# Kernel tuning notes

Measured on AMD Instinct MI355X. Metric: run time of the kernel, lower is better.

## Reference

```python
import jax, jax.numpy as jnp
import numpy as np

B, T, E, H = 2, 2048, 1024, 16
D = E // H  # head_dim = 64


def setup_inputs() -> dict:
    key = jax.random.key(0)
    ks = jax.random.split(key, 9)
    s = 0.02
    x = jax.random.normal(ks[0], (B, T, E), dtype=jnp.float32)
    # additive causal mask, broadcastable to (B, H, T, T)
    causal = jnp.tril(jnp.ones((T, T), dtype=bool))
    uni_causal_mask = jnp.where(causal, 0.0, -1e9).astype(jnp.float32)[None, None]
    # torch Linear weights are (out_features, in_features); out = H*D, in = D
    Wq = jax.random.normal(ks[1], (H * D, D), dtype=jnp.float32) * s
    bq = jax.random.normal(ks[2], (H * D,), dtype=jnp.float32) * s
    Wk = jax.random.normal(ks[3], (H * D, D), dtype=jnp.float32) * s
    bk = jax.random.normal(ks[4], (H * D,), dtype=jnp.float32) * s
    Wv = jax.random.normal(ks[5], (H * D, D), dtype=jnp.float32) * s
    bv = jax.random.normal(ks[6], (H * D,), dtype=jnp.float32) * s
    Wp = jax.random.normal(ks[7], (E, E), dtype=jnp.float32) * s
    bp = jax.random.normal(ks[8], (E,), dtype=jnp.float32) * s
    return {"x": x, "uni_causal_mask": uni_causal_mask,
            "Wq": Wq, "bq": bq, "Wk": Wk, "bk": bk,
            "Wv": Wv, "bv": bv, "Wp": Wp, "bp": bp}


def _per_head_proj(xh, W, b):
    # xh: (B, T, H, D). Original code projects each head's D-dim slice with
    # Linear(D, H*D) and get_head_dim keeps only the diagonal block i for
    # head i, i.e. each head uses W[i*D:(i+1)*D, :] and b[i*D:(i+1)*D].
    W3 = W.reshape(H, D, D)  # (H, out D, in D)
    b2 = b.reshape(H, D)
    y = jnp.einsum('bthi,hoi->bhto', xh, W3) + b2[None, :, None, :]
    return y  # (B, H, T, D)


def reference(x, uni_causal_mask, Wq, bq, Wk, bk, Wv, bv, Wp, bp):
    b, t, e = x.shape
    xh = x.reshape(b, t, H, D)
    q = _per_head_proj(xh, Wq, bq)  # (B,H,T,D)
    k = _per_head_proj(xh, Wk, bk)
    v = _per_head_proj(xh, Wv, bv)
    scale = D ** (-0.5)
    attn = jnp.einsum('bhtd,bhsd->bhts', (q * scale).astype(jnp.float32),
                      k.astype(jnp.float32))
    attn = attn + uni_causal_mask
    attn = jax.nn.softmax(attn, axis=-1).astype(x.dtype)
    out = jnp.einsum('bhts,bhsd->bhtd', attn, v)
    out = out.transpose(0, 2, 1, 3).reshape(b, t, e)
    return out @ Wp.T + bp
```

## Files before the change

### kernel.cpp

```cpp
#include <hip/hip_runtime.h>

typedef __attribute__((ext_vector_type(4))) float f32x4;
typedef __attribute__((ext_vector_type(8))) __bf16 bf16x8;
typedef __attribute__((ext_vector_type(4))) unsigned short us4;
typedef __attribute__((ext_vector_type(8))) unsigned short us8;

#define DEVI static __device__ __forceinline__

constexpr int T_ = 2048, E_ = 1024, H_ = 16, D_ = 64;
#define QSCALE (0.125f * 1.44269504088896f)

DEVI unsigned short f2b(float f) {
  union { __bf16 b; unsigned short u; } c; c.b = (__bf16)f; return c.u;
}

DEVI unsigned pkw(float a, float b) {
  union { __bf16 h[2]; unsigned u; } c;
  c.h[0] = (__bf16)a; c.h[1] = (__bf16)b; return c.u;
}

#if __has_builtin(__builtin_amdgcn_exp2f)
DEVI float fexp2(float x) { return __builtin_amdgcn_exp2f(x); }
#else
DEVI float fexp2(float x) { return __expf(x * 0.69314718056f); }
#endif

DEVI f32x4 mfma16(bf16x8 a, bf16x8 b, f32x4 c) {
  return __builtin_amdgcn_mfma_f32_16x16x32_bf16(a, b, c, 0, 0, 0);
}

__launch_bounds__(256)
__global__ void cvt_kernel(const float* __restrict__ Wq,
                           const float* __restrict__ Wk,
                           const float* __restrict__ Wv,
                           const float* __restrict__ Wp,
                           unsigned short* __restrict__ wqb,
                           unsigned short* __restrict__ wkb,
                           unsigned short* __restrict__ wvb,
                           unsigned short* __restrict__ wpb)
{
  int blk = blockIdx.x;
  const float* src; unsigned short* dst; float s = 1.0f;
  if (blk < 64)       { src = Wq; dst = wqb; s = QSCALE; }
  else if (blk < 128) { src = Wk; dst = wkb; blk -= 64; }
  else if (blk < 192) { src = Wv; dst = wvb; blk -= 128; }
  else                { src = Wp; dst = wpb; blk -= 192; }
  int i = blk * 256 + threadIdx.x;
  float4 v = *(const float4*)(src + (size_t)i * 4);
  us4 o; o[0] = f2b(v.x * s); o[1] = f2b(v.y * s); o[2] = f2b(v.z * s); o[3] = f2b(v.w * s);
  *(us4*)(dst + (size_t)i * 4) = o;
}

__launch_bounds__(256)
__global__ void qkv_kernel(const float* __restrict__ x,
                           const unsigned short* __restrict__ wqb,
                           const float* __restrict__ bq,
                           const unsigned short* __restrict__ wkb,
                           const float* __restrict__ bk,
                           const unsigned short* __restrict__ wvb,
                           const float* __restrict__ bv,
                           unsigned short* __restrict__ qo,
                           unsigned short* __restrict__ ko,
                           unsigned short* __restrict__ vto)
{
  const int bh = blockIdx.x;
  const int b  = bh >> 4;
  const int h  = bh & (H_ - 1);
  const int t0 = blockIdx.y * 128;
  __shared__ unsigned short Xl[128][72];
  const int tid = threadIdx.x;

  #pragma unroll
  for (int p = 0; p < 8; ++p) {
    int idx = p * 256 + tid;
    int row = idx >> 4, c4 = idx & 15;
    float4 v = *(const float4*)(x + ((size_t)(b * T_ + t0 + row)) * E_ + h * 64 + c4 * 4);
    us4 o; o[0] = f2b(v.x); o[1] = f2b(v.y); o[2] = f2b(v.z); o[3] = f2b(v.w);
    *(us4*)&Xl[row][c4 * 4] = o;
  }
  __syncthreads();

  const int w = tid >> 6, lane = tid & 63, lo = lane & 15, g = lane >> 4;
  const int tl0 = w * 32;

  bf16x8 xb[2][2];
  #pragma unroll
  for (int tt = 0; tt < 2; ++tt)
    #pragma unroll
    for (int kd = 0; kd < 2; ++kd)
      xb[tt][kd] = *(const bf16x8*)&Xl[tl0 + tt * 16 + lo][kd * 32 + g * 8];

  #pragma unroll
  for (int tsel = 0; tsel < 2; ++tsel) {
    const float* bias = tsel ? bk : bq;
    unsigned short* outp = tsel ? ko : qo;
    const unsigned short* wsrc = (tsel ? wkb : wqb) + (size_t)h * 4096;
    const float bs = tsel ? 1.0f : QSCALE;
    #pragma unroll
    for (int ot = 0; ot < 4; ++ot) {
      bf16x8 a0 = *(const bf16x8*)(wsrc + (ot * 16 + lo) * 64 + g * 8);
      bf16x8 a1 = *(const bf16x8*)(wsrc + (ot * 16 + lo) * 64 + 32 + g * 8);
      float4 bv4 = *(const float4*)(bias + h * 64 + ot * 16 + g * 4);
      float bb[4] = {bv4.x * bs, bv4.y * bs, bv4.z * bs, bv4.w * bs};
      #pragma unroll
      for (int tt = 0; tt < 2; ++tt) {
        f32x4 acc = {0.f, 0.f, 0.f, 0.f};
        acc = mfma16(a0, xb[tt][0], acc);
        acc = mfma16(a1, xb[tt][1], acc);
        int tg = t0 + tl0 + tt * 16 + lo;
        us4 pk;
        #pragma unroll
        for (int r = 0; r < 4; ++r) pk[r] = f2b(acc[r] + bb[r]);
        *(us4*)(outp + ((size_t)(bh * T_ + tg)) * 64 + ot * 16 + g * 4) = pk;
      }
    }
  }

  {
    const unsigned short* wsrc2 = wvb + (size_t)h * 4096;
    #pragma unroll
    for (int rt = 0; rt < 2; ++rt) {
      bf16x8 a0 = *(const bf16x8*)&Xl[tl0 + rt * 16 + lo][g * 8];
      bf16x8 a1 = *(const bf16x8*)&Xl[tl0 + rt * 16 + lo][32 + g * 8];
      #pragma unroll
      for (int ct = 0; ct < 4; ++ct) {
        bf16x8 b0 = *(const bf16x8*)(wsrc2 + (ct * 16 + lo) * 64 + g * 8);
        bf16x8 b1 = *(const bf16x8*)(wsrc2 + (ct * 16 + lo) * 64 + 32 + g * 8);
        f32x4 acc = {0.f, 0.f, 0.f, 0.f};
        acc = mfma16(a0, b0, acc);
        acc = mfma16(a1, b1, acc);
        int d = ct * 16 + lo;
        float bvs = bv[h * 64 + d];
        int tg = t0 + tl0 + rt * 16 + g * 4;
        us4 pk;
        #pragma unroll
        for (int r = 0; r < 4; ++r) pk[r] = f2b(acc[r] + bvs);
        *(us4*)(vto + ((size_t)(bh * 64 + d)) * T_ + tg) = pk;
      }
    }
  }
}

__launch_bounds__(256)
__global__ void flash_kernel(const unsigned short* __restrict__ q,
                             const unsigned short* __restrict__ kk_,
                             const unsigned short* __restrict__ vt,
                             unsigned short* __restrict__ ao)
{
  const int bh = blockIdx.x;
  const int b = bh >> 4, h = bh & 15;
  const int qt = 31 - blockIdx.y;
  const int t0 = qt * 64;
  __shared__ unsigned short Kl[2][64][64];
  __shared__ unsigned short Vl[3][64][64];
  const int tid = threadIdx.x, w = tid >> 6, lane = tid & 63, lo = lane & 15, g = lane >> 4;
  const int rs = lo & 7;

  const int srow = tid >> 3, sgi = tid & 7;
  const int khalf = (srow >> 2) & 1;
  const int gsrc = (srow >> 3) ^ (khalf << 1);
  const int prow = khalf * 16 + gsrc * 4 + (srow & 3);
  const int kkey = (sgi ^ (prow & 7)) * 8;
  const int vkey = (sgi ^ (srow & 7)) * 8;
  const unsigned short* kbase = kk_ + ((size_t)bh * T_ + srow) * 64 + sgi * 8;
  const unsigned short* vrow0 = vt + ((size_t)(bh * 64 + srow)) * T_;
  const unsigned short* vrow1 = vrow0 + (size_t)32 * T_;
  const int vco0 = sgi * 8;
  const int vco1 = ((sgi ^ 2) * 8) + 4;

  const int tw = t0 + w * 16;

  bf16x8 qf[2];
  const unsigned short* qb = q + ((size_t)(bh * T_ + tw + lo)) * 64;
  #pragma unroll
  for (int kd = 0; kd < 2; ++kd)
    qf[kd] = *(const bf16x8*)(qb + kd * 32 + g * 8);

  const int sb0 = g * 8, sb1 = ((g ^ 2) * 8) + 4;

  union { unsigned u[4]; bf16x8 v; } onec;
  onec.u[0] = onec.u[1] = onec.u[2] = onec.u[3] = 0x3f803f80u;
  const bf16x8 onesv = onec.v;

  float m_ = -1e30f;
  f32x4 zero4 = {0.f, 0.f, 0.f, 0.f};
  f32x4 lacc = zero4;
  f32x4 oacc[4];
  #pragma unroll
  for (int dt = 0; dt < 4; ++dt) oacc[dt] = zero4;

  const int nsteps = qt + 1;
  union u8c { us4 h4[2]; us8 v; };
  us8 kr0 = *(const us8*)(kbase);
  us8 kr1 = *(const us8*)(kbase + 2048);
  u8c vr0, vr1;
  vr0.h4[0] = *(const us4*)(vrow0 + vco0);
  vr0.h4[1] = *(const us4*)(vrow0 + vco1);
  vr1.h4[0] = *(const us4*)(vrow1 + vco0);
  vr1.h4[1] = *(const us4*)(vrow1 + vco1);
  *(us8*)&Kl[0][prow][kkey] = kr0;
  *(us8*)&Kl[0][prow + 32][kkey] = kr1;
  *(us8*)&Vl[0][srow][vkey] = vr0.v;
  *(us8*)&Vl[0][srow + 32][vkey] = vr1.v;
  if (nsteps > 1) {
    kr0 = *(const us8*)(kbase + 4096);
    kr1 = *(const us8*)(kbase + 4096 + 2048);
    vr0.h4[0] = *(const us4*)(vrow0 + 64 + vco0);
    vr0.h4[1] = *(const us4*)(vrow0 + 64 + vco1);
    vr1.h4[0] = *(const us4*)(vrow1 + 64 + vco0);
    vr1.h4[1] = *(const us4*)(vrow1 + 64 + vco1);
  }
  __syncthreads();

  bf16x8 pb[2];
  int vprev = 0;

  for (int stp = 0; stp < nsteps; ++stp) {
    const int cur = stp & 1;
    us8 nk0, nk1;
    u8c nv0, nv1;
    const bool pf = (stp + 2 < nsteps);
    if (pf) {
      const size_t ko_ = (size_t)(stp + 2) * 4096;
      const int so = (stp + 2) * 64;
      nk0 = *(const us8*)(kbase + ko_);
      nk1 = *(const us8*)(kbase + ko_ + 2048);
      nv0.h4[0] = *(const us4*)(vrow0 + so + vco0);
      nv0.h4[1] = *(const us4*)(vrow0 + so + vco1);
      nv1.h4[0] = *(const us4*)(vrow1 + so + vco0);
      nv1.h4[1] = *(const us4*)(vrow1 + so + vco1);
    }
    f32x4 sacc[4];
    #pragma unroll
    for (int ss = 0; ss < 4; ++ss) sacc[ss] = zero4;
    __builtin_amdgcn_s_setprio(1);
    #pragma unroll
    for (int ss = 0; ss < 4; ++ss) {
      bf16x8 ka0 = *(const bf16x8*)&Kl[cur][ss * 16 + lo][(g ^ rs) * 8];
      bf16x8 ka1 = *(const bf16x8*)&Kl[cur][ss * 16 + lo][((g | 4) ^ rs) * 8];
      sacc[ss] = mfma16(ka0, qf[0], sacc[ss]);
      sacc[ss] = mfma16(ka1, qf[1], sacc[ss]);
    }
    if (stp > 0) {
      #pragma unroll
      for (int kh = 0; kh < 2; ++kh) {
        #pragma unroll
        for (int dt = 0; dt < 4; ++dt) {
          bf16x8 va = *(const bf16x8*)&Vl[vprev][dt * 16 + lo][((kh * 4 + g) ^ rs) * 8];
          oacc[dt] = mfma16(va, pb[kh], oacc[dt]);
        }
      }
    }
    __builtin_amdgcn_s_setprio(0);
    if (stp == nsteps - 1) {
      #pragma unroll
      for (int ss = 0; ss < 4; ++ss) {
        const int sb = ((ss & 1) ? sb1 : sb0) + (ss >> 1) * 32;
        #pragma unroll
        for (int r = 0; r < 4; ++r) {
          if (t0 + sb + r > tw + lo) sacc[ss][r] = -1e30f;
        }
      }
    }
    float mx = -1e30f;
    #pragma unroll
    for (int ss = 0; ss < 4; ++ss) {
      float a = fmaxf(sacc[ss][0], sacc[ss][1]);
      float c = fmaxf(sacc[ss][2], sacc[ss][3]);
      mx = fmaxf(mx, fmaxf(a, c));
    }
    if (!__all(mx <= m_ + 8.0f)) {
      mx = fmaxf(mx, __shfl_xor(mx, 16));
      mx = fmaxf(mx, __shfl_xor(mx, 32));
      float mn = fmaxf(m_, mx);
      float corr = fexp2(m_ - mn);
      m_ = mn;
      lacc *= corr;
      #pragma unroll
      for (int dt = 0; dt < 4; ++dt) oacc[dt] *= corr;
    }
    #pragma unroll
    for (int kh = 0; kh < 2; ++kh) {
      union { unsigned u[4]; bf16x8 v; } pbc;
      #pragma unroll
      for (int half2 = 0; half2 < 2; ++half2) {
        const int ss = kh * 2 + half2;
        float p0 = fexp2(sacc[ss][0] - m_);
        float p1 = fexp2(sacc[ss][1] - m_);
        float p2 = fexp2(sacc[ss][2] - m_);
        float p3 = fexp2(sacc[ss][3] - m_);
        pbc.u[half2 * 2]     = pkw(p0, p1);
        pbc.u[half2 * 2 + 1] = pkw(p2, p3);
      }
      pb[kh] = pbc.v;
      lacc = mfma16(onesv, pb[kh], lacc);
    }
    vprev = stp % 3;
    if (stp + 1 < nsteps) {
      *(us8*)&Kl[cur ^ 1][prow][kkey] = kr0;
      *(us8*)&Kl[cur ^ 1][prow + 32][kkey] = kr1;
      const int vn = (stp + 1) % 3;
      *(us8*)&Vl[vn][srow][vkey] = vr0.v;
      *(us8*)&Vl[vn][srow + 32][vkey] = vr1.v;
    }
    __syncthreads();
    if (pf) { kr0 = nk0; kr1 = nk1; vr0 = nv0; vr1 = nv1; }
  }
  __builtin_amdgcn_s_setprio(1);
  #pragma unroll
  for (int kh = 0; kh < 2; ++kh) {
    #pragma unroll
    for (int dt = 0; dt < 4; ++dt) {
      bf16x8 va = *(const bf16x8*)&Vl[vprev][dt * 16 + lo][((kh * 4 + g) ^ rs) * 8];
      oacc[dt] = mfma16(va, pb[kh], oacc[dt]);
    }
  }
  __builtin_amdgcn_s_setprio(0);
  float inv = 1.0f / lacc[0];
  unsigned short* op = ao + ((size_t)(b * T_ + tw + lo)) * E_ + h * 64;
  #pragma unroll
  for (int dt = 0; dt < 4; ++dt) {
    us4 pk;
    #pragma unroll
    for (int r = 0; r < 4; ++r) pk[r] = f2b(oacc[dt][r] * inv);
    *(us4*)(op + dt * 16 + g * 4) = pk;
  }
}

__launch_bounds__(256)
__global__ void proj_kernel(const unsigned short* __restrict__ ao,
                            const unsigned short* __restrict__ wpb,
                            const float* __restrict__ bp,
                            float* __restrict__ out)
{
  const int bid = blockIdx.x;
  const int xcd = bid & 7, idx = bid >> 3;
  const int m0 = (xcd * 4 + (idx & 3)) * 128;
  const int n0 = (idx >> 2) * 64;
  __shared__ unsigned short Al[2][128][72];
  __shared__ unsigned short Bl[2][64][72];
  const int tid = threadIdx.x, w = tid >> 6, lane = tid & 63, lo = lane & 15, g = lane >> 4;
  const int wr = (w >> 1) * 64, wc = (w & 1) * 32;
  f32x4 zero4 = {0.f, 0.f, 0.f, 0.f};
  f32x4 acc[4][2];
  #pragma unroll
  for (int i = 0; i < 4; ++i)
    #pragma unroll
    for (int j = 0; j < 2; ++j) acc[i][j] = zero4;

  const int arow = tid >> 1, acol = (tid & 1) * 32;
  const int brow = tid >> 2, bcol = (tid & 3) * 16;
  const unsigned short* abase = ao + (size_t)(m0 + arow) * 1024 + acol;
  const unsigned short* bbase = wpb + (size_t)(n0 + brow) * 1024 + bcol;

  us8 a0, a1, a2, a3, b0, b1;
  a0 = *(const us8*)(abase);
  a1 = *(const us8*)(abase + 8);
  a2 = *(const us8*)(abase + 16);
// ... 58 lines not shown
    if (pf) { a0 = na0; a1 = na1; a2 = na2; a3 = na3; b0 = nb0; b1 = nb1; }
  }
  #pragma unroll
  for (int j = 0; j < 2; ++j) {
    int n = n0 + wc + j * 16 + lo;
    float bias = bp[n];
    #pragma unroll
    for (int i = 0; i < 4; ++i) {
      #pragma unroll
      for (int r = 0; r < 4; ++r)
        out[(size_t)(m0 + wr + i * 16 + g * 4 + r) * 1024 + n] = acc[i][j][r] + bias;
    }
  }
}

extern "C" void kernel_launch(void* const* d_in, const int* in_sizes, int n_in,
                              void* d_out, int out_size, void* d_ws, size_t ws_size,
                              hipStream_t stream)
{
  const float* x  = (const float*)d_in[0];
  const float* Wq = (const float*)d_in[2];
  const float* bq = (const float*)d_in[3];
  const float* Wk = (const float*)d_in[4];
  const float* bk = (const float*)d_in[5];
  const float* Wv = (const float*)d_in[6];
  const float* bv = (const float*)d_in[7];
  const float* Wp = (const float*)d_in[8];
  const float* bp = (const float*)d_in[9];
  float* out = (float*)d_out;

  char* ws = (char*)d_ws;
  const size_t SZ = (size_t)2 * 16 * 2048 * 64 * 2;
  unsigned short* q   = (unsigned short*)(ws);
  unsigned short* kb  = (unsigned short*)(ws + SZ);
  unsigned short* vt  = (unsigned short*)(ws + 2 * SZ);
  unsigned short* ao  = (unsigned short*)(ws + 3 * SZ);
  unsigned short* wpb = (unsigned short*)(ws + 4 * SZ);
  unsigned short* wqb = (unsigned short*)(ws + 4 * SZ + 2097152);
  unsigned short* wkb = wqb + 65536;
  unsigned short* wvb = wqb + 131072;

  cvt_kernel<<<dim3(1216), 256, 0, stream>>>(Wq, Wk, Wv, Wp, wqb, wkb, wvb, wpb);
  qkv_kernel<<<dim3(32, 16), 256, 0, stream>>>(x, wqb, bq, wkb, bk, wvb, bv, q, kb, vt);
  flash_kernel<<<dim3(32, 32), 256, 0, stream>>>(q, kb, vt, ao);
  proj_kernel<<<dim3(512), 256, 0, stream>>>(ao, wpb, bp, out);
}
```

Baseline: 78.53 us.

## Pre-swizzle K/V tiles in QKV kernel and load them via direct global-to-LDS

The QKV kernel now writes K and V^T in a tile-major, pre-swizzled layout that matches the flash kernel's LDS layout. The flash kernel can then fetch whole 8 KB tiles with global_load_lds 16-byte copies, with no register staging or LDS stores. The flash block shrinks to 2 waves, each handling 32 query rows (two 16-row tiles), so every K/V LDS read feeds twice as many MFMAs. The cost is more registers per wave and fewer waves per block. The causal mask is now applied per wave based on tile overlap rather than only on the last step.

```diff
diff --git a/kernel.cpp b/kernel.cpp
--- a/kernel.cpp
+++ b/kernel.cpp
@@ -27,6 +27,12 @@
 
 DEVI f32x4 mfma16(bf16x8 a, bf16x8 b, f32x4 c) {
   return __builtin_amdgcn_mfma_f32_16x16x32_bf16(a, b, c, 0, 0, 0);
+}
+
+DEVI void gl16(const void* g, void* l) {
+  __builtin_amdgcn_global_load_lds(
+      (const __attribute__((address_space(1))) unsigned int*)g,
+      (__attribute__((address_space(3))) unsigned int*)l, 16, 0, 0);
 }
 
 __launch_bounds__(256)
@@ -60,8 +66,8 @@
                            const unsigned short* __restrict__ wvb,
                            const float* __restrict__ bv,
                            unsigned short* __restrict__ qo,
-                           unsigned short* __restrict__ ko,
-                           unsigned short* __restrict__ vto)
+                           unsigned short* __restrict__ kb2,
+                           unsigned short* __restrict__ vt2)
 {
   const int bh = blockIdx.x;
   const int b  = bh >> 4;
@@ -93,7 +99,6 @@
   #pragma unroll
   for (int tsel = 0; tsel < 2; ++tsel) {
     const float* bias = tsel ? bk : bq;
-    unsigned short* outp = tsel ? ko : qo;
     const unsigned short* wsrc = (tsel ? wkb : wqb) + (size_t)h * 4096;
     const float bs = tsel ? 1.0f : QSCALE;
     #pragma unroll
@@ -111,7 +116,18 @@
         us4 pk;
         #pragma unroll
         for (int r = 0; r < 4; ++r) pk[r] = f2b(acc[r] + bb[r]);
-        *(us4*)(outp + ((size_t)(bh * T_ + tg)) * 64 + ot * 16 + g * 4) = pk;
+        if (tsel == 0) {
+          *(us4*)(qo + ((size_t)(bh * T_ + tg)) * 64 + ot * 16 + g * 4) = pk;
+        } else {
+          const int s6 = tg & 63;
+          const int s5 = s6 & 31, h32 = s6 >> 5;
+          const int kh2 = (s5 >> 2) & 1;
+          const int gs = ((s5 >> 3) ^ (kh2 << 1)) & 3;
+          const int p = h32 * 32 + kh2 * 16 + gs * 4 + (s5 & 3);
+          const int gl = ot * 2 + (g >> 1);
+          const int gphys = gl ^ (p & 7);
+          *(us4*)(kb2 + (size_t)bh * 131072 + (tg >> 6) * 4096 + p * 64 + gphys * 8 + (g & 1) * 4) = pk;
+        }
       }
     }
   }
@@ -129,22 +145,26 @@
         f32x4 acc = {0.f, 0.f, 0.f, 0.f};
         acc = mfma16(a0, b0, acc);
         acc = mfma16(a1, b1, acc);
-        int d = ct * 16 + lo;
+        const int d = ct * 16 + lo;
         float bvs = bv[h * 64 + d];
-        int tg = t0 + tl0 + rt * 16 + g * 4;
+        const int tg = t0 + tl0 + rt * 16 + g * 4;
         us4 pk;
         #pragma unroll
         for (int r = 0; r < 4; ++r) pk[r] = f2b(acc[r] + bvs);
-        *(us4*)(vto + ((size_t)(bh * 64 + d)) * T_ + tg) = pk;
-      }
-    }
-  }
-}
-
-__launch_bounds__(256)
+        const int lg = (tg & 63) >> 3;
+        const int nib = g & 1;
+        const int sgi2 = nib ? (lg ^ 2) : lg;
+        const int pv = sgi2 ^ (d & 7);
+        *(us4*)(vt2 + (size_t)bh * 131072 + (tg >> 6) * 4096 + d * 64 + pv * 8 + nib * 4) = pk;
+      }
+    }
+  }
+}
+
+__launch_bounds__(128)
 __global__ void flash_kernel(const unsigned short* __restrict__ q,
-                             const unsigned short* __restrict__ kk_,
-                             const unsigned short* __restrict__ vt,
+                             const unsigned short* __restrict__ kb2,
+                             const unsigned short* __restrict__ vt2,
                              unsigned short* __restrict__ ao)
 {
   const int bh = blockIdx.x;
@@ -156,25 +176,21 @@
   const int tid = threadIdx.x, w = tid >> 6, lane = tid & 63, lo = lane & 15, g = lane >> 4;
   const int rs = lo & 7;
 
-  const int srow = tid >> 3, sgi = tid & 7;
-  const int khalf = (srow >> 2) & 1;
-  const int gsrc = (srow >> 3) ^ (khalf << 1);
-  const int prow = khalf * 16 + gsrc * 4 + (srow & 3);
-  const int kkey = (sgi ^ (prow & 7)) * 8;
-  const int vkey = (sgi ^ (srow & 7)) * 8;
-  const unsigned short* kbase = kk_ + ((size_t)bh * T_ + srow) * 64 + sgi * 8;
-  const unsigned short* vrow0 = vt + ((size_t)(bh * 64 + srow)) * T_;
-  const unsigned short* vrow1 = vrow0 + (size_t)32 * T_;
-  const int vco0 = sgi * 8;
-  const int vco1 = ((sgi ^ 2) * 8) + 4;
-
-  const int tw = t0 + w * 16;
-
-  bf16x8 qf[2];
-  const unsigned short* qb = q + ((size_t)(bh * T_ + tw + lo)) * 64;
-  #pragma unroll
-  for (int kd = 0; kd < 2; ++kd)
-    qf[kd] = *(const bf16x8*)(qb + kd * 32 + g * 8);
+  const char* ksrc = (const char*)kb2 + (size_t)bh * 262144;
+  const char* vsrc = (const char*)vt2 + (size_t)bh * 262144;
+  const int loff = w * 4096 + lane * 16;
+  const int wbase = w * 4096;
+
+  const int tw = t0 + w * 32;
+
+  bf16x8 qf[2][2];
+  #pragma unroll
+  for (int tt = 0; tt < 2; ++tt) {
+    const unsigned short* qb = q + ((size_t)(bh * T_ + tw + tt * 16 + lo)) * 64;
+    #pragma unroll
+    for (int kd = 0; kd < 2; ++kd)
+      qf[tt][kd] = *(const bf16x8*)(qb + kd * 32 + g * 8);
+  }
 
   const int sb0 = g * 8, sb1 = ((g ^ 2) * 8) + 4;
 
@@ -182,64 +198,59 @@
   onec.u[0] = onec.u[1] = onec.u[2] = onec.u[3] = 0x3f803f80u;
   const bf16x8 onesv = onec.v;
 
-  float m_ = -1e30f;
+  float m_[2] = {-1e30f, -1e30f};
   f32x4 zero4 = {0.f, 0.f, 0.f, 0.f};
-  f32x4 lacc = zero4;
-  f32x4 oacc[4];
-  #pragma unroll
-  for (int dt = 0; dt < 4; ++dt) oacc[dt] = zero4;
+  f32x4 lacc[2] = {zero4, zero4};
+  f32x4 oacc[4][2];
+  #pragma unroll
+  for (int dt = 0; dt < 4; ++dt)
+    #pragma unroll
+    for (int tt = 0; tt < 2; ++tt) oacc[dt][tt] = zero4;
 
   const int nsteps = qt + 1;
-  union u8c { us4 h4[2]; us8 v; };
-  us8 kr0 = *(const us8*)(kbase);
-  us8 kr1 = *(const us8*)(kbase + 2048);
-  u8c vr0, vr1;
-  vr0.h4[0] = *(const us4*)(vrow0 + vco0);
-  vr0.h4[1] = *(const us4*)(vrow0 + vco1);
-  vr1.h4[0] = *(const us4*)(vrow1 + vco0);
-  vr1.h4[1] = *(const us4*)(vrow1 + vco1);
-  *(us8*)&Kl[0][prow][kkey] = kr0;
-  *(us8*)&Kl[0][prow + 32][kkey] = kr1;
-  *(us8*)&Vl[0][srow][vkey] = vr0.v;
-  *(us8*)&Vl[0][srow + 32][vkey] = vr1.v;
-  if (nsteps > 1) {
-    kr0 = *(const us8*)(kbase + 4096);
-    kr1 = *(const us8*)(kbase + 4096 + 2048);
-    vr0.h4[0] = *(const us4*)(vrow0 + 64 + vco0);
-    vr0.h4[1] = *(const us4*)(vrow0 + 64 + vco1);
-    vr1.h4[0] = *(const us4*)(vrow1 + 64 + vco0);
-    vr1.h4[1] = *(const us4*)(vrow1 + 64 + vco1);
+  {
+    const char* ks = ksrc + loff;
+    const char* vs = vsrc + loff;
+    char* kd = (char*)&Kl[0][0][0] + wbase;
+    char* vd = (char*)&Vl[0][0][0] + wbase;
+    gl16(ks, kd); gl16(ks + 1024, kd + 1024);
+    gl16(ks + 2048, kd + 2048); gl16(ks + 3072, kd + 3072);
+    gl16(vs, vd); gl16(vs + 1024, vd + 1024);
+    gl16(vs + 2048, vd + 2048); gl16(vs + 3072, vd + 3072);
   }
   __syncthreads();
 
-  bf16x8 pb[2];
+  bf16x8 pb[2][2];
   int vprev = 0;
 
   for (int stp = 0; stp < nsteps; ++stp) {
     const int cur = stp & 1;
-    us8 nk0, nk1;
-    u8c nv0, nv1;
-    const bool pf = (stp + 2 < nsteps);
-    if (pf) {
-      const size_t ko_ = (size_t)(stp + 2) * 4096;
-      const int so = (stp + 2) * 64;
-      nk0 = *(const us8*)(kbase + ko_);
-      nk1 = *(const us8*)(kbase + ko_ + 2048);
-      nv0.h4[0] = *(const us4*)(vrow0 + so + vco0);
-      nv0.h4[1] = *(const us4*)(vrow0 + so + vco1);
-      nv1.h4[0] = *(const us4*)(vrow1 + so + vco0);
-      nv1.h4[1] = *(const us4*)(vrow1 + so + vco1);
-    }
-    f32x4 sacc[4];
-    #pragma unroll
-    for (int ss = 0; ss < 4; ++ss) sacc[ss] = zero4;
+    const int s0 = stp * 64;
+    if (stp + 1 < nsteps) {
+      const char* ks = ksrc + (size_t)(stp + 1) * 8192 + loff;
+      const char* vs = vsrc + (size_t)(stp + 1) * 8192 + loff;
+      char* kd = (char*)&Kl[cur ^ 1][0][0] + wbase;
+      char* vd = (char*)&Vl[(stp + 1) % 3][0][0] + wbase;
+      gl16(ks, kd); gl16(ks + 1024, kd + 1024);
+      gl16(ks + 2048, kd + 2048); gl16(ks + 3072, kd + 3072);
+      gl16(vs, vd); gl16(vs + 1024, vd + 1024);
+      gl16(vs + 2048, vd + 2048); gl16(vs + 3072, vd + 3072);
+    }
+    f32x4 sacc[4][2];
+    #pragma unroll
+    for (int ss = 0; ss < 4; ++ss)
+      #pragma unroll
+      for (int tt = 0; tt < 2; ++tt) sacc[ss][tt] = zero4;
     __builtin_amdgcn_s_setprio(1);
     #pragma unroll
     for (int ss = 0; ss < 4; ++ss) {
       bf16x8 ka0 = *(const bf16x8*)&Kl[cur][ss * 16 + lo][(g ^ rs) * 8];
       bf16x8 ka1 = *(const bf16x8*)&Kl[cur][ss * 16 + lo][((g | 4) ^ rs) * 8];
-      sacc[ss] = mfma16(ka0, qf[0], sacc[ss]);
-      sacc[ss] = mfma16(ka1, qf[1], sacc[ss]);
+      #pragma unroll
+      for (int tt = 0; tt < 2; ++tt) {
+        sacc[ss][tt] = mfma16(ka0, qf[tt][0], sacc[ss][tt]);
+        sacc[ss][tt] = mfma16(ka1, qf[tt][1], sacc[ss][tt]);
+      }
     }
     if (stp > 0) {
       #pragma unroll
@@ -247,64 +258,71 @@
         #pragma unroll
         for (int dt = 0; dt < 4; ++dt) {
           bf16x8 va = *(const bf16x8*)&Vl[vprev][dt * 16 + lo][((kh * 4 + g) ^ rs) * 8];
-          oacc[dt] = mfma16(va, pb[kh], oacc[dt]);
+          #pragma unroll
+          for (int tt = 0; tt < 2; ++tt)
+            oacc[dt][tt] = mfma16(va, pb[tt][kh], oacc[dt][tt]);
         }
       }
     }
     __builtin_amdgcn_s_setprio(0);
-    if (stp == nsteps - 1) {
+    if (s0 + 63 > tw) {
       #pragma unroll
       for (int ss = 0; ss < 4; ++ss) {
-        const int sb = ((ss & 1) ? sb1 : sb0) + (ss >> 1) * 32;
-        #pragma unroll
-        for (int r = 0; r < 4; ++r) {
-          if (t0 + sb + r > tw + lo) sacc[ss][r] = -1e30f;
+        const int sb = s0 + ((ss & 1) ? sb1 : sb0) + (ss >> 1) * 32;
+        #pragma unroll
+        for (int tt = 0; tt < 2; ++tt) {
+          const int tg = tw + tt * 16 + lo;
+          #pragma unroll
+          for (int r = 0; r < 4; ++r) {
+            if (sb + r > tg) sacc[ss][tt][r] = -1e30f;
+          }
         }
       }
     }
-    float mx = -1e30f;
-    #pragma unroll
-    for (int ss = 0; ss < 4; ++ss) {
-      float a = fmaxf(sacc[ss][0], sacc[ss][1]);
-      float c = fmaxf(sacc[ss][2], sacc[ss][3]);
-      mx = fmaxf(mx, fmaxf(a, c));
-    }
-    if (!__all(mx <= m_ + 8.0f)) {
-      mx = fmaxf(mx, __shfl_xor(mx, 16));
-      mx = fmaxf(mx, __shfl_xor(mx, 32));
-      float mn = fmaxf(m_, mx);
-      float corr = fexp2(m_ - mn);
-      m_ = mn;
-      lacc *= corr;
-      #pragma unroll
-      for (int dt = 0; dt < 4; ++dt) oacc[dt] *= corr;
-    }
-    #pragma unroll
-    for (int kh = 0; kh < 2; ++kh) {
-      union { unsigned u[4]; bf16x8 v; } pbc;
-      #pragma unroll
-      for (int half2 = 0; half2 < 2; ++half2) {
-        const int ss = kh * 2 + half2;
-        float p0 = fexp2(sacc[ss][0] - m_);
-        float p1 = fexp2(sacc[ss][1] - m_);
-        float p2 = fexp2(sacc[ss][2] - m_);
-        float p3 = fexp2(sacc[ss][3] - m_);
-        pbc.u[half2 * 2]     = pkw(p0, p1);
-        pbc.u[half2 * 2 + 1] = pkw(p2, p3);
-      }
-      pb[kh] = pbc.v;
-      lacc = mfma16(onesv, pb[kh], lacc);
+    float mx[2];
+    #pragma unroll
+    for (int tt = 0; tt < 2; ++tt) {
+      float a = fmaxf(fmaxf(sacc[0][tt][0], sacc[0][tt][1]), fmaxf(sacc[0][tt][2], sacc[0][tt][3]));
+      float b2 = fmaxf(fmaxf(sacc[1][tt][0], sacc[1][tt][1]), fmaxf(sacc[1][tt][2], sacc[1][tt][3]));
+      float c = fmaxf(fmaxf(sacc[2][tt][0], sacc[2][tt][1]), fmaxf(sacc[2][tt][2], sacc[2][tt][3]));
+      float d = fmaxf(fmaxf(sacc[3][tt][0], sacc[3][tt][1]), fmaxf(sacc[3][tt][2], sacc[3][tt][3]));
+      mx[tt] = fmaxf(fmaxf(a, b2), fmaxf(c, d));
+    }
+    if (!__all((mx[0] <= m_[0] + 8.0f) && (mx[1] <= m_[1] + 8.0f))) {
+      #pragma unroll
+      for (int tt = 0; tt < 2; ++tt) {
+        float mv = mx[tt];
+        mv = fmaxf(mv, __shfl_xor(mv, 16));
+        mv = fmaxf(mv, __shfl_xor(mv, 32));
+        float mn = fmaxf(m_[tt], mv);
+        float corr = fexp2(m_[tt] - mn);
+        m_[tt] = mn;
+        lacc[tt] *= corr;
+        #pragma unroll
+        for (int dt = 0; dt < 4; ++dt) oacc[dt][tt] *= corr;
+      }
+    }
+    #pragma unroll
+    for (int tt = 0; tt < 2; ++tt) {
+      #pragma unroll
+      for (int kh = 0; kh < 2; ++kh) {
+        union { unsigned u[4]; bf16x8 v; } pbc;
+        #pragma unroll
+        for (int half2 = 0; half2 < 2; ++half2) {
+          const int ss = kh * 2 + half2;
+          float p0 = fexp2(sacc[ss][tt][0] - m_[tt]);
+          float p1 = fexp2(sacc[ss][tt][1] - m_[tt]);
+          float p2 = fexp2(sacc[ss][tt][2] - m_[tt]);
+          float p3 = fexp2(sacc[ss][tt][3] - m_[tt]);
+          pbc.u[half2 * 2]     = pkw(p0, p1);
+          pbc.u[half2 * 2 + 1] = pkw(p2, p3);
+        }
+        pb[tt][kh] = pbc.v;
+        lacc[tt] = mfma16(onesv, pb[tt][kh], lacc[tt]);
+      }
     }
     vprev = stp % 3;
-    if (stp + 1 < nsteps) {
-      *(us8*)&Kl[cur ^ 1][prow][kkey] = kr0;
-      *(us8*)&Kl[cur ^ 1][prow + 32][kkey] = kr1;
-      const int vn = (stp + 1) % 3;
-      *(us8*)&Vl[vn][srow][vkey] = vr0.v;
-      *(us8*)&Vl[vn][srow + 32][vkey] = vr1.v;
-    }
     __syncthreads();
-    if (pf) { kr0 = nk0; kr1 = nk1; vr0 = nv0; vr1 = nv1; }
   }
   __builtin_amdgcn_s_setprio(1);
   #pragma unroll
@@ -312,18 +330,23 @@
     #pragma unroll
     for (int dt = 0; dt < 4; ++dt) {
       bf16x8 va = *(const bf16x8*)&Vl[vprev][dt * 16 + lo][((kh * 4 + g) ^ rs) * 8];
-      oacc[dt] = mfma16(va, pb[kh], oacc[dt]);
+      #pragma unroll
+      for (int tt = 0; tt < 2; ++tt)
+        oacc[dt][tt] = mfma16(va, pb[tt][kh], oacc[dt][tt]);
     }
   }
   __builtin_amdgcn_s_setprio(0);
-  float inv = 1.0f / lacc[0];
-  unsigned short* op = ao + ((size_t)(b * T_ + tw + lo)) * E_ + h * 64;
-  #pragma unroll
-  for (int dt = 0; dt < 4; ++dt) {
-    us4 pk;
-    #pragma unroll
-    for (int r = 0; r < 4; ++r) pk[r] = f2b(oacc[dt][r] * inv);
-    *(us4*)(op + dt * 16 + g * 4) = pk;
+  #pragma unroll
+  for (int tt = 0; tt < 2; ++tt) {
+    float inv = 1.0f / lacc[tt][0];
+    unsigned short* op = ao + ((size_t)(b * T_ + tw + tt * 16 + lo)) * E_ + h * 64;
+    #pragma unroll
+    for (int dt = 0; dt < 4; ++dt) {
+      us4 pk;
+      #pragma unroll
+      for (int r = 0; r < 4; ++r) pk[r] = f2b(oacc[dt][tt][r] * inv);
+      *(us4*)(op + dt * 16 + g * 4) = pk;
+    }
   }
 }
 
@@ -448,8 +471,8 @@
   char* ws = (char*)d_ws;
   const size_t SZ = (size_t)2 * 16 * 2048 * 64 * 2;
   unsigned short* q   = (unsigned short*)(ws);
-  unsigned short* kb  = (unsigned short*)(ws + SZ);
-  unsigned short* vt  = (unsigned short*)(ws + 2 * SZ);
+  unsigned short* kb2 = (unsigned short*)(ws + SZ);
+  unsigned short* vt2 = (unsigned short*)(ws + 2 * SZ);
   unsigned short* ao  = (unsigned short*)(ws + 3 * SZ);
   unsigned short* wpb = (unsigned short*)(ws + 4 * SZ);
   unsigned short* wqb = (unsigned short*)(ws + 4 * SZ + 2097152);
@@ -457,7 +480,7 @@
   unsigned short* wvb = wqb + 131072;
 
   cvt_kernel<<<dim3(1216), 256, 0, stream>>>(Wq, Wk, Wv, Wp, wqb, wkb, wvb, wpb);
-  qkv_kernel<<<dim3(32, 16), 256, 0, stream>>>(x, wqb, bq, wkb, bk, wvb, bv, q, kb, vt);
-  flash_kernel<<<dim3(32, 32), 256, 0, stream>>>(q, kb, vt, ao);
+  qkv_kernel<<<dim3(32, 16), 256, 0, stream>>>(x, wqb, bq, wkb, bk, wvb, bv, q, kb2, vt2);
+  flash_kernel<<<dim3(32, 32), 128, 0, stream>>>(q, kb2, vt2, ao);
   proj_kernel<<<dim3(512), 256, 0, stream>>>(ao, wpb, bp, out);
 }
```

Measured after the change: 88.70 us. 1.13x slower.

## Process two batch-head pairs per flash attention block to halve grid size

Applied to the files above, without the earlier changes.

Each flash attention block now handles the same head and query tile for both batch elements, interleaving two independent online-softmax streams with doubled K/V shared buffers and register state. The grid shrinks from 1024 blocks to 512. The aim is more independent MFMA work per barrier, which hides latency and amortizes the per-step synchronisation. The cost is double the LDS (about 80KB) and many more registers, which lowers occupancy, and fewer blocks to balance the uneven causal workload.

```diff
diff --git a/kernel.cpp b/kernel.cpp
--- a/kernel.cpp
+++ b/kernel.cpp
@@ -147,12 +147,12 @@
                              const unsigned short* __restrict__ vt,
                              unsigned short* __restrict__ ao)
 {
-  const int bh = blockIdx.x;
-  const int b = bh >> 4, h = bh & 15;
-  const int qt = 31 - blockIdx.y;
+  const int id = blockIdx.x;
+  const int pr = id & 15;
+  const int qt = 31 - (id >> 4);
   const int t0 = qt * 64;
-  __shared__ unsigned short Kl[2][64][64];
-  __shared__ unsigned short Vl[3][64][64];
+  __shared__ unsigned short Kl[2][2][64][64];
+  __shared__ unsigned short Vl[2][3][64][64];
   const int tid = threadIdx.x, w = tid >> 6, lane = tid & 63, lo = lane & 15, g = lane >> 4;
   const int rs = lo & 7;
 
@@ -162,19 +162,31 @@
   const int prow = khalf * 16 + gsrc * 4 + (srow & 3);
   const int kkey = (sgi ^ (prow & 7)) * 8;
   const int vkey = (sgi ^ (srow & 7)) * 8;
-  const unsigned short* kbase = kk_ + ((size_t)bh * T_ + srow) * 64 + sgi * 8;
-  const unsigned short* vrow0 = vt + ((size_t)(bh * 64 + srow)) * T_;
-  const unsigned short* vrow1 = vrow0 + (size_t)32 * T_;
   const int vco0 = sgi * 8;
   const int vco1 = ((sgi ^ 2) * 8) + 4;
 
+  const unsigned short* kbase[2];
+  const unsigned short* vrow0[2];
+  const unsigned short* vrow1[2];
+  #pragma unroll
+  for (int pp = 0; pp < 2; ++pp) {
+    const int bh = pr + pp * 16;
+    kbase[pp] = kk_ + ((size_t)bh * T_ + srow) * 64 + sgi * 8;
+    vrow0[pp] = vt + ((size_t)(bh * 64 + srow)) * T_;
+    vrow1[pp] = vrow0[pp] + (size_t)32 * T_;
+  }
+
   const int tw = t0 + w * 16;
 
-  bf16x8 qf[2];
-  const unsigned short* qb = q + ((size_t)(bh * T_ + tw + lo)) * 64;
-  #pragma unroll
-  for (int kd = 0; kd < 2; ++kd)
-    qf[kd] = *(const bf16x8*)(qb + kd * 32 + g * 8);
+  bf16x8 qf[2][2];
+  #pragma unroll
+  for (int pp = 0; pp < 2; ++pp) {
+    const int bh = pr + pp * 16;
+    const unsigned short* qb = q + ((size_t)(bh * T_ + tw + lo)) * 64;
+    #pragma unroll
+    for (int kd = 0; kd < 2; ++kd)
+      qf[pp][kd] = *(const bf16x8*)(qb + kd * 32 + g * 8);
+  }
 
   const int sb0 = g * 8, sb1 = ((g ^ 2) * 8) + 4;
 
@@ -182,148 +194,185 @@
   onec.u[0] = onec.u[1] = onec.u[2] = onec.u[3] = 0x3f803f80u;
   const bf16x8 onesv = onec.v;
 
-  float m_ = -1e30f;
+  float m_[2] = {-1e30f, -1e30f};
   f32x4 zero4 = {0.f, 0.f, 0.f, 0.f};
-  f32x4 lacc = zero4;
-  f32x4 oacc[4];
-  #pragma unroll
-  for (int dt = 0; dt < 4; ++dt) oacc[dt] = zero4;
+  f32x4 lacc[2] = {zero4, zero4};
+  f32x4 oacc[2][4];
+  #pragma unroll
+  for (int pp = 0; pp < 2; ++pp)
+    #pragma unroll
+    for (int dt = 0; dt < 4; ++dt) oacc[pp][dt] = zero4;
 
   const int nsteps = qt + 1;
   union u8c { us4 h4[2]; us8 v; };
-  us8 kr0 = *(const us8*)(kbase);
-  us8 kr1 = *(const us8*)(kbase + 2048);
-  u8c vr0, vr1;
-  vr0.h4[0] = *(const us4*)(vrow0 + vco0);
-  vr0.h4[1] = *(const us4*)(vrow0 + vco1);
-  vr1.h4[0] = *(const us4*)(vrow1 + vco0);
-  vr1.h4[1] = *(const us4*)(vrow1 + vco1);
-  *(us8*)&Kl[0][prow][kkey] = kr0;
-  *(us8*)&Kl[0][prow + 32][kkey] = kr1;
-  *(us8*)&Vl[0][srow][vkey] = vr0.v;
-  *(us8*)&Vl[0][srow + 32][vkey] = vr1.v;
+  us8 kr0[2], kr1[2];
+  u8c vr0[2], vr1[2];
+  #pragma unroll
+  for (int pp = 0; pp < 2; ++pp) {
+    kr0[pp] = *(const us8*)(kbase[pp]);
+    kr1[pp] = *(const us8*)(kbase[pp] + 2048);
+    vr0[pp].h4[0] = *(const us4*)(vrow0[pp] + vco0);
+    vr0[pp].h4[1] = *(const us4*)(vrow0[pp] + vco1);
+    vr1[pp].h4[0] = *(const us4*)(vrow1[pp] + vco0);
+    vr1[pp].h4[1] = *(const us4*)(vrow1[pp] + vco1);
+    *(us8*)&Kl[pp][0][prow][kkey] = kr0[pp];
+    *(us8*)&Kl[pp][0][prow + 32][kkey] = kr1[pp];
+    *(us8*)&Vl[pp][0][srow][vkey] = vr0[pp].v;
+    *(us8*)&Vl[pp][0][srow + 32][vkey] = vr1[pp].v;
+  }
   if (nsteps > 1) {
-    kr0 = *(const us8*)(kbase + 4096);
-    kr1 = *(const us8*)(kbase + 4096 + 2048);
-    vr0.h4[0] = *(const us4*)(vrow0 + 64 + vco0);
-    vr0.h4[1] = *(const us4*)(vrow0 + 64 + vco1);
-    vr1.h4[0] = *(const us4*)(vrow1 + 64 + vco0);
-    vr1.h4[1] = *(const us4*)(vrow1 + 64 + vco1);
+    #pragma unroll
+    for (int pp = 0; pp < 2; ++pp) {
+      kr0[pp] = *(const us8*)(kbase[pp] + 4096);
+      kr1[pp] = *(const us8*)(kbase[pp] + 4096 + 2048);
+      vr0[pp].h4[0] = *(const us4*)(vrow0[pp] + 64 + vco0);
+      vr0[pp].h4[1] = *(const us4*)(vrow0[pp] + 64 + vco1);
+      vr1[pp].h4[0] = *(const us4*)(vrow1[pp] + 64 + vco0);
+      vr1[pp].h4[1] = *(const us4*)(vrow1[pp] + 64 + vco1);
+    }
   }
   __syncthreads();
 
-  bf16x8 pb[2];
+  bf16x8 pb[2][2];
   int vprev = 0;
 
   for (int stp = 0; stp < nsteps; ++stp) {
     const int cur = stp & 1;
-    us8 nk0, nk1;
-    u8c nv0, nv1;
+    us8 nk0[2], nk1[2];
+    u8c nv0[2], nv1[2];
     const bool pf = (stp + 2 < nsteps);
     if (pf) {
       const size_t ko_ = (size_t)(stp + 2) * 4096;
       const int so = (stp + 2) * 64;
-      nk0 = *(const us8*)(kbase + ko_);
-      nk1 = *(const us8*)(kbase + ko_ + 2048);
-      nv0.h4[0] = *(const us4*)(vrow0 + so + vco0);
-      nv0.h4[1] = *(const us4*)(vrow0 + so + vco1);
-      nv1.h4[0] = *(const us4*)(vrow1 + so + vco0);
-      nv1.h4[1] = *(const us4*)(vrow1 + so + vco1);
-    }
-    f32x4 sacc[4];
-    #pragma unroll
-    for (int ss = 0; ss < 4; ++ss) sacc[ss] = zero4;
+      #pragma unroll
+      for (int pp = 0; pp < 2; ++pp) {
+        nk0[pp] = *(const us8*)(kbase[pp] + ko_);
+        nk1[pp] = *(const us8*)(kbase[pp] + ko_ + 2048);
+        nv0[pp].h4[0] = *(const us4*)(vrow0[pp] + so + vco0);
+        nv0[pp].h4[1] = *(const us4*)(vrow0[pp] + so + vco1);
+        nv1[pp].h4[0] = *(const us4*)(vrow1[pp] + so + vco0);
+        nv1[pp].h4[1] = *(const us4*)(vrow1[pp] + so + vco1);
+      }
+    }
+    f32x4 sacc[2][4];
+    #pragma unroll
+    for (int pp = 0; pp < 2; ++pp)
+      #pragma unroll
+      for (int ss = 0; ss < 4; ++ss) sacc[pp][ss] = zero4;
     __builtin_amdgcn_s_setprio(1);
     #pragma unroll
-    for (int ss = 0; ss < 4; ++ss) {
-      bf16x8 ka0 = *(const bf16x8*)&Kl[cur][ss * 16 + lo][(g ^ rs) * 8];
-      bf16x8 ka1 = *(const bf16x8*)&Kl[cur][ss * 16 + lo][((g | 4) ^ rs) * 8];
-      sacc[ss] = mfma16(ka0, qf[0], sacc[ss]);
-      sacc[ss] = mfma16(ka1, qf[1], sacc[ss]);
+    for (int pp = 0; pp < 2; ++pp) {
+      #pragma unroll
+      for (int ss = 0; ss < 4; ++ss) {
+        bf16x8 ka0 = *(const bf16x8*)&Kl[pp][cur][ss * 16 + lo][(g ^ rs) * 8];
+        bf16x8 ka1 = *(const bf16x8*)&Kl[pp][cur][ss * 16 + lo][((g | 4) ^ rs) * 8];
+        sacc[pp][ss] = mfma16(ka0, qf[pp][0], sacc[pp][ss]);
+        sacc[pp][ss] = mfma16(ka1, qf[pp][1], sacc[pp][ss]);
+      }
     }
     if (stp > 0) {
       #pragma unroll
-      for (int kh = 0; kh < 2; ++kh) {
-        #pragma unroll
-        for (int dt = 0; dt < 4; ++dt) {
-          bf16x8 va = *(const bf16x8*)&Vl[vprev][dt * 16 + lo][((kh * 4 + g) ^ rs) * 8];
-          oacc[dt] = mfma16(va, pb[kh], oacc[dt]);
-        }
-      }
+      for (int pp = 0; pp < 2; ++pp)
+        #pragma unroll
+        for (int kh = 0; kh < 2; ++kh)
+          #pragma unroll
+          for (int dt = 0; dt < 4; ++dt) {
+            bf16x8 va = *(const bf16x8*)&Vl[pp][vprev][dt * 16 + lo][((kh * 4 + g) ^ rs) * 8];
+            oacc[pp][dt] = mfma16(va, pb[pp][kh], oacc[pp][dt]);
+          }
     }
     __builtin_amdgcn_s_setprio(0);
     if (stp == nsteps - 1) {
       #pragma unroll
+      for (int pp = 0; pp < 2; ++pp)
+        #pragma unroll
+        for (int ss = 0; ss < 4; ++ss) {
+          const int sb = ((ss & 1) ? sb1 : sb0) + (ss >> 1) * 32;
+          #pragma unroll
+          for (int r = 0; r < 4; ++r) {
+            if (t0 + sb + r > tw + lo) sacc[pp][ss][r] = -1e30f;
+          }
+        }
+    }
+    #pragma unroll
+    for (int pp = 0; pp < 2; ++pp) {
+      float mx = -1e30f;
+      #pragma unroll
       for (int ss = 0; ss < 4; ++ss) {
-        const int sb = ((ss & 1) ? sb1 : sb0) + (ss >> 1) * 32;
-        #pragma unroll
-        for (int r = 0; r < 4; ++r) {
-          if (t0 + sb + r > tw + lo) sacc[ss][r] = -1e30f;
+        float a = fmaxf(sacc[pp][ss][0], sacc[pp][ss][1]);
+        float c = fmaxf(sacc[pp][ss][2], sacc[pp][ss][3]);
+        mx = fmaxf(mx, fmaxf(a, c));
+      }
+      if (!__all(mx <= m_[pp] + 8.0f)) {
+        mx = fmaxf(mx, __shfl_xor(mx, 16));
+        mx = fmaxf(mx, __shfl_xor(mx, 32));
+        float mn = fmaxf(m_[pp], mx);
+        float corr = fexp2(m_[pp] - mn);
+        m_[pp] = mn;
+        lacc[pp] *= corr;
+        #pragma unroll
+        for (int dt = 0; dt < 4; ++dt) oacc[pp][dt] *= corr;
+      }
+      #pragma unroll
+      for (int kh = 0; kh < 2; ++kh) {
+        union { unsigned u[4]; bf16x8 v; } pbc;
+        #pragma unroll
+        for (int half2 = 0; half2 < 2; ++half2) {
+          const int ss = kh * 2 + half2;
+          float p0 = fexp2(sacc[pp][ss][0] - m_[pp]);
+          float p1 = fexp2(sacc[pp][ss][1] - m_[pp]);
+          float p2 = fexp2(sacc[pp][ss][2] - m_[pp]);
+          float p3 = fexp2(sacc[pp][ss][3] - m_[pp]);
+          pbc.u[half2 * 2]     = pkw(p0, p1);
+          pbc.u[half2 * 2 + 1] = pkw(p2, p3);
         }
-      }
-    }
-    float mx = -1e30f;
-    #pragma unroll
-    for (int ss = 0; ss < 4; ++ss) {
-      float a = fmaxf(sacc[ss][0], sacc[ss][1]);
-      float c = fmaxf(sacc[ss][2], sacc[ss][3]);
-      mx = fmaxf(mx, fmaxf(a, c));
-    }
-    if (!__all(mx <= m_ + 8.0f)) {
-      mx = fmaxf(mx, __shfl_xor(mx, 16));
-      mx = fmaxf(mx, __shfl_xor(mx, 32));
-      float mn = fmaxf(m_, mx);
-      float corr = fexp2(m_ - mn);
-      m_ = mn;
-      lacc *= corr;
-      #pragma unroll
-      for (int dt = 0; dt < 4; ++dt) oacc[dt] *= corr;
-    }
-    #pragma unroll
-    for (int kh = 0; kh < 2; ++kh) {
-      union { unsigned u[4]; bf16x8 v; } pbc;
-      #pragma unroll
-      for (int half2 = 0; half2 < 2; ++half2) {
-        const int ss = kh * 2 + half2;
-        float p0 = fexp2(sacc[ss][0] - m_);
-        float p1 = fexp2(sacc[ss][1] - m_);
-        float p2 = fexp2(sacc[ss][2] - m_);
-        float p3 = fexp2(sacc[ss][3] - m_);
-        pbc.u[half2 * 2]     = pkw(p0, p1);
-        pbc.u[half2 * 2 + 1] = pkw(p2, p3);
-      }
-      pb[kh] = pbc.v;
-      lacc = mfma16(onesv, pb[kh], lacc);
+        pb[pp][kh] = pbc.v;
+        lacc[pp] = mfma16(onesv, pb[pp][kh], lacc[pp]);
+      }
     }
     vprev = stp % 3;
     if (stp + 1 < nsteps) {
-      *(us8*)&Kl[cur ^ 1][prow][kkey] = kr0;
-      *(us8*)&Kl[cur ^ 1][prow + 32][kkey] = kr1;
       const int vn = (stp + 1) % 3;
-      *(us8*)&Vl[vn][srow][vkey] = vr0.v;
-      *(us8*)&Vl[vn][srow + 32][vkey] = vr1.v;
+      #pragma unroll
+      for (int pp = 0; pp < 2; ++pp) {
+        *(us8*)&Kl[pp][cur ^ 1][prow][kkey] = kr0[pp];
+        *(us8*)&Kl[pp][cur ^ 1][prow + 32][kkey] = kr1[pp];
+        *(us8*)&Vl[pp][vn][srow][vkey] = vr0[pp].v;
+        *(us8*)&Vl[pp][vn][srow + 32][vkey] = vr1[pp].v;
+      }
     }
     __syncthreads();
-    if (pf) { kr0 = nk0; kr1 = nk1; vr0 = nv0; vr1 = nv1; }
+    if (pf) {
+      #pragma unroll
+      for (int pp = 0; pp < 2; ++pp) {
+        kr0[pp] = nk0[pp]; kr1[pp] = nk1[pp];
+        vr0[pp] = nv0[pp]; vr1[pp] = nv1[pp];
+      }
+    }
   }
   __builtin_amdgcn_s_setprio(1);
   #pragma unroll
-  for (int kh = 0; kh < 2; ++kh) {
+  for (int pp = 0; pp < 2; ++pp)
+    #pragma unroll
+    for (int kh = 0; kh < 2; ++kh)
+      #pragma unroll
+      for (int dt = 0; dt < 4; ++dt) {
+        bf16x8 va = *(const bf16x8*)&Vl[pp][vprev][dt * 16 + lo][((kh * 4 + g) ^ rs) * 8];
+        oacc[pp][dt] = mfma16(va, pb[pp][kh], oacc[pp][dt]);
+      }
+  __builtin_amdgcn_s_setprio(0);
+  #pragma unroll
+  for (int pp = 0; pp < 2; ++pp) {
+    const int b = pp, h = pr;
+    float inv = 1.0f / lacc[pp][0];
+    unsigned short* op = ao + ((size_t)(b * T_ + tw + lo)) * E_ + h * 64;
     #pragma unroll
     for (int dt = 0; dt < 4; ++dt) {
-      bf16x8 va = *(const bf16x8*)&Vl[vprev][dt * 16 + lo][((kh * 4 + g) ^ rs) * 8];
-      oacc[dt] = mfma16(va, pb[kh], oacc[dt]);
-    }
-  }
-  __builtin_amdgcn_s_setprio(0);
-  float inv = 1.0f / lacc[0];
-  unsigned short* op = ao + ((size_t)(b * T_ + tw + lo)) * E_ + h * 64;
-  #pragma unroll
-  for (int dt = 0; dt < 4; ++dt) {
-    us4 pk;
-    #pragma unroll
-    for (int r = 0; r < 4; ++r) pk[r] = f2b(oacc[dt][r] * inv);
-    *(us4*)(op + dt * 16 + g * 4) = pk;
+      us4 pk;
+      #pragma unroll
+      for (int r = 0; r < 4; ++r) pk[r] = f2b(oacc[pp][dt][r] * inv);
+      *(us4*)(op + dt * 16 + g * 4) = pk;
+    }
   }
 }
 
@@ -458,6 +507,6 @@
 
   cvt_kernel<<<dim3(1216), 256, 0, stream>>>(Wq, Wk, Wv, Wp, wqb, wkb, wvb, wpb);
   qkv_kernel<<<dim3(32, 16), 256, 0, stream>>>(x, wqb, bq, wkb, bk, wvb, bv, q, kb, vt);
-  flash_kernel<<<dim3(32, 32), 256, 0, stream>>>(q, kb, vt, ao);
+  flash_kernel<<<dim3(512), 256, 0, stream>>>(q, kb, vt, ao);
   proj_kernel<<<dim3(512), 256, 0, stream>>>(ao, wpb, bp, out);
 }
```

New measurement: 98.32 us. 25.2% more time.

## Process two KV tiles per barrier with deeper LDS ring buffers in flash kernel

Applied to the files above, without the earlier changes.

Restructures the flash attention main loop to handle two 64-key steps per __syncthreads, using 4 K buffers and 5 V buffers in LDS arranged as rings. Global loads for the next two tiles are issued at the top of each iteration and written to LDS after both steps. This halves the number of block barriers and deepens prefetch. In exchange LDS use grows from 20KB to 36KB, which may lower occupancy, and register pressure rises from holding two tiles of prefetched data.

```diff
diff --git a/kernel.cpp b/kernel.cpp
--- a/kernel.cpp
+++ b/kernel.cpp
@@ -151,8 +151,8 @@
   const int b = bh >> 4, h = bh & 15;
   const int qt = 31 - blockIdx.y;
   const int t0 = qt * 64;
-  __shared__ unsigned short Kl[2][64][64];
-  __shared__ unsigned short Vl[3][64][64];
+  __shared__ unsigned short Kl[4][64][64];
+  __shared__ unsigned short Vl[5][64][64];
   const int tid = threadIdx.x, w = tid >> 6, lane = tid & 63, lo = lane & 15, g = lane >> 4;
   const int rs = lo & 7;
 
@@ -191,68 +191,32 @@
 
   const int nsteps = qt + 1;
   union u8c { us4 h4[2]; us8 v; };
-  us8 kr0 = *(const us8*)(kbase);
-  us8 kr1 = *(const us8*)(kbase + 2048);
-  u8c vr0, vr1;
-  vr0.h4[0] = *(const us4*)(vrow0 + vco0);
-  vr0.h4[1] = *(const us4*)(vrow0 + vco1);
-  vr1.h4[0] = *(const us4*)(vrow1 + vco0);
-  vr1.h4[1] = *(const us4*)(vrow1 + vco1);
-  *(us8*)&Kl[0][prow][kkey] = kr0;
-  *(us8*)&Kl[0][prow + 32][kkey] = kr1;
-  *(us8*)&Vl[0][srow][vkey] = vr0.v;
-  *(us8*)&Vl[0][srow + 32][vkey] = vr1.v;
-  if (nsteps > 1) {
-    kr0 = *(const us8*)(kbase + 4096);
-    kr1 = *(const us8*)(kbase + 4096 + 2048);
-    vr0.h4[0] = *(const us4*)(vrow0 + 64 + vco0);
-    vr0.h4[1] = *(const us4*)(vrow0 + 64 + vco1);
-    vr1.h4[0] = *(const us4*)(vrow1 + 64 + vco0);
-    vr1.h4[1] = *(const us4*)(vrow1 + 64 + vco1);
-  }
-  __syncthreads();
-
   bf16x8 pb[2];
-  int vprev = 0;
-
-  for (int stp = 0; stp < nsteps; ++stp) {
-    const int cur = stp & 1;
-    us8 nk0, nk1;
-    u8c nv0, nv1;
-    const bool pf = (stp + 2 < nsteps);
-    if (pf) {
-      const size_t ko_ = (size_t)(stp + 2) * 4096;
-      const int so = (stp + 2) * 64;
-      nk0 = *(const us8*)(kbase + ko_);
-      nk1 = *(const us8*)(kbase + ko_ + 2048);
-      nv0.h4[0] = *(const us4*)(vrow0 + so + vco0);
-      nv0.h4[1] = *(const us4*)(vrow0 + so + vco1);
-      nv1.h4[0] = *(const us4*)(vrow1 + so + vco0);
-      nv1.h4[1] = *(const us4*)(vrow1 + so + vco1);
-    }
+
+  auto step_body = [&](int I, int KB, int VPB) {
     f32x4 sacc[4];
     #pragma unroll
     for (int ss = 0; ss < 4; ++ss) sacc[ss] = zero4;
     __builtin_amdgcn_s_setprio(1);
     #pragma unroll
     for (int ss = 0; ss < 4; ++ss) {
-      bf16x8 ka0 = *(const bf16x8*)&Kl[cur][ss * 16 + lo][(g ^ rs) * 8];
-      bf16x8 ka1 = *(const bf16x8*)&Kl[cur][ss * 16 + lo][((g | 4) ^ rs) * 8];
+      bf16x8 ka0 = *(const bf16x8*)&Kl[KB][ss * 16 + lo][(g ^ rs) * 8];
+      bf16x8 ka1 = *(const bf16x8*)&Kl[KB][ss * 16 + lo][((g | 4) ^ rs) * 8];
       sacc[ss] = mfma16(ka0, qf[0], sacc[ss]);
       sacc[ss] = mfma16(ka1, qf[1], sacc[ss]);
     }
-    if (stp > 0) {
+    if (I > 0) {
       #pragma unroll
       for (int kh = 0; kh < 2; ++kh) {
         #pragma unroll
         for (int dt = 0; dt < 4; ++dt) {
-          bf16x8 va = *(const bf16x8*)&Vl[vprev][dt * 16 + lo][((kh * 4 + g) ^ rs) * 8];
+          bf16x8 va = *(const bf16x8*)&Vl[VPB][dt * 16 + lo][((kh * 4 + g) ^ rs) * 8];
           oacc[dt] = mfma16(va, pb[kh], oacc[dt]);
         }
       }
     }
     __builtin_amdgcn_s_setprio(0);
-    if (stp == nsteps - 1) {
+    if (I == nsteps - 1) {
       #pragma unroll
       for (int ss = 0; ss < 4; ++ss) {
         const int sb = ((ss & 1) ? sb1 : sb0) + (ss >> 1) * 32;
@@ -295,23 +259,95 @@
       pb[kh] = pbc.v;
       lacc = mfma16(onesv, pb[kh], lacc);
     }
-    vprev = stp % 3;
-    if (stp + 1 < nsteps) {
-      *(us8*)&Kl[cur ^ 1][prow][kkey] = kr0;
-      *(us8*)&Kl[cur ^ 1][prow + 32][kkey] = kr1;
-      const int vn = (stp + 1) % 3;
-      *(us8*)&Vl[vn][srow][vkey] = vr0.v;
-      *(us8*)&Vl[vn][srow + 32][vkey] = vr1.v;
+  };
+
+  {
+    us8 k0 = *(const us8*)(kbase);
+    us8 k1 = *(const us8*)(kbase + 2048);
+    u8c v0, v1;
+    v0.h4[0] = *(const us4*)(vrow0 + vco0);
+    v0.h4[1] = *(const us4*)(vrow0 + vco1);
+    v1.h4[0] = *(const us4*)(vrow1 + vco0);
+    v1.h4[1] = *(const us4*)(vrow1 + vco1);
+    *(us8*)&Kl[0][prow][kkey] = k0;
+    *(us8*)&Kl[0][prow + 32][kkey] = k1;
+    *(us8*)&Vl[0][srow][vkey] = v0.v;
+    *(us8*)&Vl[0][srow + 32][vkey] = v1.v;
+    if (nsteps > 1) {
+      k0 = *(const us8*)(kbase + 4096);
+      k1 = *(const us8*)(kbase + 4096 + 2048);
+      v0.h4[0] = *(const us4*)(vrow0 + 64 + vco0);
+      v0.h4[1] = *(const us4*)(vrow0 + 64 + vco1);
+      v1.h4[0] = *(const us4*)(vrow1 + 64 + vco0);
+      v1.h4[1] = *(const us4*)(vrow1 + 64 + vco1);
+      *(us8*)&Kl[1][prow][kkey] = k0;
+      *(us8*)&Kl[1][prow + 32][kkey] = k1;
+      *(us8*)&Vl[1][srow][vkey] = v0.v;
+      *(us8*)&Vl[1][srow + 32][vkey] = v1.v;
+    }
+  }
+  __syncthreads();
+
+  int v0r = 0;
+  int vlast = 0;
+
+  for (int base = 0; base < nsteps; base += 2) {
+    const int vA  = v0r;
+    const int vPA = (v0r + 4 >= 5) ? v0r - 1 : v0r + 4;
+    const int vB  = (v0r + 1 >= 5) ? v0r - 4 : v0r + 1;
+    const int vC  = (v0r + 2 >= 5) ? v0r - 3 : v0r + 2;
+    const int vD  = (v0r + 3 >= 5) ? v0r - 2 : v0r + 3;
+    const bool e2 = base + 2 < nsteps;
+    const bool e3 = base + 3 < nsteps;
+    us8 nk0a, nk1a, nk0b, nk1b;
+    u8c nv0a, nv1a, nv0b, nv1b;
+    if (e2) {
+      const size_t ko_ = (size_t)(base + 2) * 4096;
+      const int so = (base + 2) * 64;
+      nk0a = *(const us8*)(kbase + ko_);
+      nk1a = *(const us8*)(kbase + ko_ + 2048);
+      nv0a.h4[0] = *(const us4*)(vrow0 + so + vco0);
+      nv0a.h4[1] = *(const us4*)(vrow0 + so + vco1);
+      nv1a.h4[0] = *(const us4*)(vrow1 + so + vco0);
+      nv1a.h4[1] = *(const us4*)(vrow1 + so + vco1);
+    }
+    if (e3) {
+      const size_t ko_ = (size_t)(base + 3) * 4096;
+      const int so = (base + 3) * 64;
+      nk0b = *(const us8*)(kbase + ko_);
+      nk1b = *(const us8*)(kbase + ko_ + 2048);
+      nv0b.h4[0] = *(const us4*)(vrow0 + so + vco0);
+      nv0b.h4[1] = *(const us4*)(vrow0 + so + vco1);
+      nv1b.h4[0] = *(const us4*)(vrow1 + so + vco0);
+      nv1b.h4[1] = *(const us4*)(vrow1 + so + vco1);
+    }
+    step_body(base, base & 3, vPA);
+    vlast = vA;
+    if (base + 1 < nsteps) {
+      step_body(base + 1, (base + 1) & 3, vA);
+      vlast = vB;
+    }
+    if (e2) {
+      *(us8*)&Kl[(base + 2) & 3][prow][kkey] = nk0a;
+      *(us8*)&Kl[(base + 2) & 3][prow + 32][kkey] = nk1a;
+      *(us8*)&Vl[vC][srow][vkey] = nv0a.v;
+      *(us8*)&Vl[vC][srow + 32][vkey] = nv1a.v;
+    }
+    if (e3) {
+      *(us8*)&Kl[(base + 3) & 3][prow][kkey] = nk0b;
+      *(us8*)&Kl[(base + 3) & 3][prow + 32][kkey] = nk1b;
+      *(us8*)&Vl[vD][srow][vkey] = nv0b.v;
+      *(us8*)&Vl[vD][srow + 32][vkey] = nv1b.v;
     }
     __syncthreads();
-    if (pf) { kr0 = nk0; kr1 = nk1; vr0 = nv0; vr1 = nv1; }
+    v0r += 2; if (v0r >= 5) v0r -= 5;
   }
   __builtin_amdgcn_s_setprio(1);
   #pragma unroll
   for (int kh = 0; kh < 2; ++kh) {
     #pragma unroll
     for (int dt = 0; dt < 4; ++dt) {
-      bf16x8 va = *(const bf16x8*)&Vl[vprev][dt * 16 + lo][((kh * 4 + g) ^ rs) * 8];
+      bf16x8 va = *(const bf16x8*)&Vl[vlast][dt * 16 + lo][((kh * 4 + g) ^ rs) * 8];
       oacc[dt] = mfma16(va, pb[kh], oacc[dt]);
     }
   }
```

After: 79.50 us. Within noise of the previous version (+1.2%).
